# Performance work log

Measured on AMD Instinct MI355X. Metric: run time of the kernel, lower is better.

The kernel has to match this reference:

```python
import jax, jax.numpy as jnp
import numpy as np

N_NODES = 50000
N_EDGES = 800000
D_FEAT = 64
N_AGENTS = 1024
A_DIM = 16
MSG = 128          # msg_dim
OUT = 128          # out_dim


def _w(k, fan_in, fan_out):
    return jax.random.normal(k, (fan_in, fan_out), jnp.float32) / np.sqrt(fan_in).astype(np.float32)


def setup_inputs() -> dict:
    key = jax.random.key(0)
    ks = jax.random.split(key, 24)
    inp = {}
    inp["x"] = jax.random.normal(ks[0], (N_NODES, D_FEAT), jnp.float32)
    inp["actions"] = jax.random.normal(ks[1], (N_AGENTS, A_DIM), jnp.float32)
    inp["senders"] = jax.random.randint(ks[2], (N_EDGES,), 0, N_NODES, jnp.int32)
    inp["receivers"] = jax.random.randint(ks[3], (N_EDGES,), 0, N_NODES, jnp.int32)
    inp["n_agents"] = N_AGENTS
    # message MLP: concat(sender, receiver) -> 256 -> 256 -> msg_dim
    inp["W_m1"] = _w(ks[4], 2 * D_FEAT, 256); inp["b_m1"] = jnp.zeros((256,), jnp.float32)
    inp["W_m2"] = _w(ks[5], 256, 256);        inp["b_m2"] = jnp.zeros((256,), jnp.float32)
    inp["W_m3"] = _w(ks[6], 256, MSG);        inp["b_m3"] = jnp.zeros((MSG,), jnp.float32)
    # aggregation MLP: msg_dim -> 128 -> 128 -> msg_dim
    inp["W_a1"] = _w(ks[7], MSG, 128);        inp["b_a1"] = jnp.zeros((128,), jnp.float32)
    inp["W_a2"] = _w(ks[8], 128, 128);        inp["b_a2"] = jnp.zeros((128,), jnp.float32)
    inp["W_a3"] = _w(ks[9], 128, MSG);        inp["b_a3"] = jnp.zeros((MSG,), jnp.float32)
    # update MLP: concat(node, aggregated) -> 256 -> 256 -> out_dim
    inp["W_u1"] = _w(ks[10], D_FEAT + MSG, 256); inp["b_u1"] = jnp.zeros((256,), jnp.float32)
    inp["W_u2"] = _w(ks[11], 256, 256);          inp["b_u2"] = jnp.zeros((256,), jnp.float32)
    inp["W_u3"] = _w(ks[12], 256, OUT);          inp["b_u3"] = jnp.zeros((OUT,), jnp.float32)
    # critic head
    inp["W_act"] = _w(ks[13], A_DIM, 128);    inp["b_act"] = jnp.zeros((128,), jnp.float32)
    inp["W_h1"] = _w(ks[14], OUT + 128, 256); inp["b_h1"] = jnp.zeros((256,), jnp.float32)
    inp["W_h2"] = _w(ks[15], 256, 256);       inp["b_h2"] = jnp.zeros((256,), jnp.float32)
    inp["W_q"] = _w(ks[16], 256, 1);          inp["b_q"] = jnp.zeros((1,), jnp.float32)
    return inp


def reference(x, actions, senders, receivers, n_agents,
              W_m1, b_m1, W_m2, b_m2, W_m3, b_m3,
              W_a1, b_a1, W_a2, b_a2, W_a3, b_a3,
              W_u1, b_u1, W_u2, b_u2, W_u3, b_u3,
              W_act, b_act, W_h1, b_h1, W_h2, b_h2, W_q, b_q):
    relu = jax.nn.relu
    # --- GNN layer: edge messages (gather endpoints, MLP) ---
    h = jnp.concatenate([x[senders], x[receivers]], axis=-1)   # [E, 2*D]
    h = relu(h @ W_m1 + b_m1)
    h = relu(h @ W_m2 + b_m2)
    msg = h @ W_m3 + b_m3                                      # [E, MSG]
    # --- aggregate messages at receivers (scatter-add) ---
    aggr = jax.ops.segment_sum(msg, receivers, num_segments=x.shape[0])  # [N, MSG]
    a = relu(aggr @ W_a1 + b_a1)
    a = relu(a @ W_a2 + b_a2)
    a = a @ W_a3 + b_a3                                        # [N, MSG]
    # --- node update ---
    u = jnp.concatenate([x, a], axis=-1)                       # [N, D+MSG]
    u = relu(u @ W_u1 + b_u1)
    u = relu(u @ W_u2 + b_u2)
    feats = (u @ W_u3 + b_u3)[:n_agents]                       # agent (type-0) nodes
    # --- critic head ---
    ap = relu(actions @ W_act + b_act)                         # [n_agents, 128]
    z = jnp.concatenate([feats, ap], axis=-1)
    z = relu(z @ W_h1 + b_h1)
    z = relu(z @ W_h2 + b_h2)
    q = z @ W_q + b_q
    return jnp.squeeze(q, axis=-1)                             # [n_agents]
```

## Files before the change

### kernel.cpp

```cpp
#include <hip/hip_runtime.h>
#include <hip/hip_bf16.h>


#define STRIDE 260

typedef __attribute__((ext_vector_type(8))) short short8;
typedef __attribute__((ext_vector_type(4))) float floatx4;
union Frag8 { short8 s; uint u[4]; };

__device__ __forceinline__ void cvt_hi_lo(const float4 f0, const float4 f1,
                                          Frag8& hi, Frag8& lo) {
    uint U[8] = { __float_as_uint(f0.x), __float_as_uint(f0.y),
                  __float_as_uint(f0.z), __float_as_uint(f0.w),
                  __float_as_uint(f1.x), __float_as_uint(f1.y),
                  __float_as_uint(f1.z), __float_as_uint(f1.w) };
    float F[8] = { f0.x, f0.y, f0.z, f0.w, f1.x, f1.y, f1.z, f1.w };
#pragma unroll
    for (int p = 0; p < 4; ++p) {
        uint a = U[2*p], b = U[2*p+1];
        hi.u[p] = (a >> 16) | (b & 0xFFFF0000u);
        float l0 = F[2*p]   - __uint_as_float(a & 0xFFFF0000u);
        float l1 = F[2*p+1] - __uint_as_float(b & 0xFFFF0000u);
        __hip_bfloat162 pl = __float22bfloat162_rn(make_float2(l0, l1));
        union { __hip_bfloat162 h; uint v; } cvt; cvt.h = pl;
        lo.u[p] = cvt.v;
    }
}

__device__ __forceinline__ uint f2bf(float f) {
    uint u = __float_as_uint(f);
    return (u + 0x7FFFu + ((u >> 16) & 1u)) >> 16;
}
__device__ __forceinline__ float bf2f(uint h) { return __uint_as_float(h << 16); }
__device__ __forceinline__ uint split2(float f0, float f1, uint& lo) {
    uint h0 = f2bf(f0), h1 = f2bf(f1);
    uint l0 = f2bf(f0 - bf2f(h0)), l1 = f2bf(f1 - bf2f(h1));
    lo = l0 | (l1 << 16);
    return h0 | (h1 << 16);
}

constexpr int PK_NIN[11]  = {128,256,256, 128,128,128, 192,256,256, 256,256};
constexpr int PK_NOUT[11] = {256,256,128, 128,128,128, 256,256,128, 256,256};
constexpr int pk_entries(int m) { return (PK_NIN[m]/32)*(PK_NOUT[m]/16)*64; }
constexpr int pk_cum(int m) { int s = 0; for (int i = 0; i < m; ++i) s += pk_entries(i); return s; }
constexpr int PK_TOTAL = pk_cum(11);
constexpr int pk_off_hi(int m) { return 2*pk_cum(m); }
constexpr int pk_off_lo(int m) { return 2*pk_cum(m) + pk_entries(m); }

struct PackPtrs { const float* W[11]; };

#define FILT_CHUNK 4096

__global__ void pack_and_filter(PackPtrs P, uint4* __restrict__ pack,
                                const int* __restrict__ senders,
                                const int* __restrict__ receivers,
                                int E, int n_agents, int cap,
                                int* __restrict__ counter,
                                int2* __restrict__ edges, int FB) {
    __shared__ int lcount;
    __shared__ int lbase;
    __shared__ int2 lbuf[FILT_CHUNK];
    const int t = (int)threadIdx.x;
    if ((int)blockIdx.x < FB) {
        if (t == 0) lcount = 0;
        __syncthreads();
        int start = blockIdx.x * FILT_CHUNK;
        int end = min(start + FILT_CHUNK, E);
        for (int b0 = start; b0 < end; b0 += 256) {
            int idx = b0 + t;
            int r = -1, s = 0;
            bool pred = false;
            if (idx < end) {
                r = receivers[idx];
                pred = (r < n_agents);
                if (pred) s = senders[idx];
            }
            unsigned long long m = __ballot(pred);
            int lane = t & 63;
            int below = __popcll(m & ((1ull << lane) - 1));
            int cnt = __popcll(m);
            int wbase = 0;
            if (lane == 0 && cnt) wbase = atomicAdd(&lcount, cnt);
            wbase = __shfl(wbase, 0, 64);
            if (pred) lbuf[wbase + below] = make_int2(s, r);
        }
        __syncthreads();
        if (t == 0) lbase = atomicAdd(counter, lcount);
        __syncthreads();
        for (int i = t; i < lcount; i += 256) {
            int pos = lbase + i;
            if (pos < cap) edges[pos] = lbuf[i];
        }
        return;
    }
    int g = ((int)blockIdx.x - FB) * 256 + t;
    if (g >= PK_TOTAL) return;
    int m = 0;
#pragma unroll
    for (int i = 1; i < 11; ++i) if (g >= pk_cum(i)) m = i;
    int local = g - pk_cum(m);
    const float* W = P.W[m];
    int NOUT = PK_NOUT[m], NT = NOUT / 16;
    int lane = local & 63;
    int tmp  = local >> 6;
    int nt = tmp % NT, kb = tmp / NT;
    int n  = nt * 16 + (lane & 15);
    int k0 = kb * 32 + (lane >> 4) * 8;
    uint hi[4], lo[4];
#pragma unroll
    for (int p = 0; p < 4; ++p) {
        float f0 = W[(size_t)(k0 + 2*p)     * NOUT + n];
        float f1 = W[(size_t)(k0 + 2*p + 1) * NOUT + n];
        hi[p] = split2(f0, f1, lo[p]);
    }
    pack[pk_off_hi(m) + local] = make_uint4(hi[0], hi[1], hi[2], hi[3]);
    pack[pk_off_lo(m) + local] = make_uint4(lo[0], lo[1], lo[2], lo[3]);
}

template<int NIN, int NOUT, bool RELU>
__device__ __forceinline__ void mfma_layer(const float* in_lds, float* out_lds,
                                           const uint4* __restrict__ Whi,
                                           const uint4* __restrict__ Wlo,
                                           const float* __restrict__ b) {
    constexpr int KB  = NIN / 32;
    constexpr int NT  = NOUT / 16;
    constexpr int NTW = NT / 4;
    const int t    = (int)threadIdx.x;
    const int wave = t >> 6;
    const int l15  = t & 15;
    const int quad = (t >> 4) & 3;

    floatx4 acc[2][NTW];
#pragma unroll
    for (int mt = 0; mt < 2; ++mt)
#pragma unroll
        for (int i = 0; i < NTW; ++i) acc[mt][i] = (floatx4){0.f, 0.f, 0.f, 0.f};

#pragma unroll 2
    for (int kb = 0; kb < KB; ++kb) {
        Frag8 ahi[2], alo[2];
#pragma unroll
        for (int mt = 0; mt < 2; ++mt) {
            const float* src = in_lds + (mt * 16 + l15) * STRIDE + kb * 32 + quad * 8;
            float4 f0 = *(const float4*)src;
            float4 f1 = *(const float4*)(src + 4);
            cvt_hi_lo(f0, f1, ahi[mt], alo[mt]);
        }
#pragma unroll
        for (int i = 0; i < NTW; ++i) {
            int nt = wave * NTW + i;
            int widx = (kb * NT + nt) * 64 + (t & 63);
            Frag8 bhi, blo;
            *(uint4*)bhi.u = Whi[widx];
            *(uint4*)blo.u = Wlo[widx];
#pragma unroll
            for (int mt = 0; mt < 2; ++mt) {
                acc[mt][i] = __builtin_amdgcn_mfma_f32_16x16x32_bf16(alo[mt].s, bhi.s, acc[mt][i], 0, 0, 0);
                acc[mt][i] = __builtin_amdgcn_mfma_f32_16x16x32_bf16(ahi[mt].s, blo.s, acc[mt][i], 0, 0, 0);
                acc[mt][i] = __builtin_amdgcn_mfma_f32_16x16x32_bf16(ahi[mt].s, bhi.s, acc[mt][i], 0, 0, 0);
            }
        }
    }
#pragma unroll
    for (int i = 0; i < NTW; ++i) {
        int n = (wave * NTW + i) * 16 + l15;
        float bias = b[n];
#pragma unroll
        for (int mt = 0; mt < 2; ++mt) {
#pragma unroll
            for (int r = 0; r < 4; ++r) {
                float v = acc[mt][i][r] + bias;
                if (RELU) v = fmaxf(v, 0.f);
                out_lds[(mt * 16 + quad * 4 + r) * STRIDE + n] = v;
            }
        }
    }
}

template<int NIN, int NOUT, bool RELU, int OOFF>
__device__ __forceinline__ void mfma_layer16(const float* in_lds, float* out_lds,
                                             const uint4* __restrict__ Whi,
                                             const uint4* __restrict__ Wlo,
                                             const float* __restrict__ b) {
    constexpr int KB  = NIN / 32;
    constexpr int NT  = NOUT / 16;
    constexpr int NTW = NT / 4;
    const int t    = (int)threadIdx.x;
    const int wave = t >> 6;
    const int l15  = t & 15;
    const int quad = (t >> 4) & 3;

    floatx4 acc[NTW];
#pragma unroll
    for (int i = 0; i < NTW; ++i) acc[i] = (floatx4){0.f, 0.f, 0.f, 0.f};

#pragma unroll 2
    for (int kb = 0; kb < KB; ++kb) {
        Frag8 ahi, alo;
        const float* src = in_lds + l15 * STRIDE + kb * 32 + quad * 8;
        float4 f0 = *(const float4*)src;
        float4 f1 = *(const float4*)(src + 4);
        cvt_hi_lo(f0, f1, ahi, alo);
#pragma unroll
        for (int i = 0; i < NTW; ++i) {
            int widx = (kb * NT + wave * NTW + i) * 64 + (t & 63);
            Frag8 bhi, blo;
            *(uint4*)bhi.u = Whi[widx];
            *(uint4*)blo.u = Wlo[widx];
            acc[i] = __builtin_amdgcn_mfma_f32_16x16x32_bf16(alo.s, bhi.s, acc[i], 0, 0, 0);
            acc[i] = __builtin_amdgcn_mfma_f32_16x16x32_bf16(ahi.s, blo.s, acc[i], 0, 0, 0);
            acc[i] = __builtin_amdgcn_mfma_f32_16x16x32_bf16(ahi.s, bhi.s, acc[i], 0, 0, 0);
        }
    }
#pragma unroll
    for (int i = 0; i < NTW; ++i) {
        int n = (wave * NTW + i) * 16 + l15;
        float bias = b[n];
#pragma unroll
        for (int r = 0; r < 4; ++r) {
            float v = acc[i][r] + bias;
            if (RELU) v = fmaxf(v, 0.f);
            out_lds[(quad * 4 + r) * STRIDE + OOFF + n] = v;
        }
    }
}

#define ETE 32
__global__ __launch_bounds__(256, 2)
void edge_mlp(const float* __restrict__ x, const int2* __restrict__ edges,
              const int* __restrict__ counter, int cap, float* __restrict__ aggr,
              const uint4* __restrict__ pack,
              const float* __restrict__ bm1, const float* __restrict__ bm2,
              const float* __restrict__ bm3) {
    __shared__ float bufA[ETE * STRIDE];
    __shared__ float bufB[ETE * STRIDE];
    __shared__ int sL[ETE], rL[ETE];
    const uint4* W1hi = pack + pk_off_hi(0);
    const uint4* W1lo = pack + pk_off_lo(0);
    const uint4* W2hi = pack + pk_off_hi(1);
    const uint4* W2lo = pack + pk_off_lo(1);
    const uint4* W3hi = pack + pk_off_hi(2);
    const uint4* W3lo = pack + pk_off_lo(2);
    const int count = min(counter[0], cap);
    const int ntiles = (count + ETE - 1) / ETE;
    const int t = (int)threadIdx.x;
    for (int tile = (int)blockIdx.x; tile < ntiles; tile += (int)gridDim.x) {
        const int base = tile * ETE;
        if (t < ETE) {
            int eg = base + t;
            int2 ed = (eg < count) ? edges[eg] : make_int2(0, -1);
            sL[t] = ed.x; rL[t] = ed.y;
        }
        __syncthreads();
        for (int idx = t; idx < ETE * 32; idx += 256) {
            int e = idx >> 5;
            int f4 = (idx & 31) * 4;
            int node = (f4 < 64) ? sL[e] : rL[e];
            float4 v = make_float4(0.f, 0.f, 0.f, 0.f);
            if (rL[e] >= 0) v = *(const float4*)(x + (size_t)node * 64 + (f4 & 63));
            *(float4*)(bufA + e * STRIDE + f4) = v;
        }
        __syncthreads();
        mfma_layer<128, 256, true >(bufA, bufB, W1hi, W1lo, bm1);
        __syncthreads();
        mfma_layer<256, 256, true >(bufB, bufA, W2hi, W2lo, bm2);
        __syncthreads();
        mfma_layer<256, 128, false>(bufA, bufB, W3hi, W3lo, bm3);
        __syncthreads();
        for (int idx = t; idx < ETE * 128; idx += 256) {
            int e = idx >> 7, o = idx & 127;
            if (base + e < count) {
                atomicAdd(&aggr[(size_t)rL[e] * 128 + o], bufB[e * STRIDE + o]);
            }
        }
        __syncthreads();
    }
}

__global__ __launch_bounds__(256, 1)
void node_update(const float* __restrict__ x, const float* __restrict__ actions,
                 const float* __restrict__ aggr, int n_agents,
                 const uint4* __restrict__ pack,
                 const float* __restrict__ ba1, const float* __restrict__ ba2,
                 const float* __restrict__ ba3,
                 const float* __restrict__ bu1, const float* __restrict__ bu2,
                 const float* __restrict__ bu3,
                 const float* __restrict__ Wact, const float* __restrict__ bact,
                 const float* __restrict__ bh1, const float* __restrict__ bh2,
                 const float* __restrict__ Wq,  const float* __restrict__ bq,
                 float* __restrict__ out) {
    __shared__ float bufA[16 * STRIDE];
    __shared__ float bufB[16 * STRIDE];
    __shared__ float qpart[16][17];
    const int t = (int)threadIdx.x;
    const int base = (int)blockIdx.x * 16;

    for (int idx = t; idx < 16 * 32; idx += 256) {
        int e = idx >> 5, f4 = (idx & 31) * 4;
        float4 v = make_float4(0.f, 0.f, 0.f, 0.f);
        if (base + e < n_agents) v = *(const float4*)(aggr + (size_t)(base + e) * 128 + f4);
        *(float4*)(bufA + e * STRIDE + f4) = v;
    }
    __syncthreads();
    mfma_layer16<128, 128, true,  0 >(bufA, bufB, pack + pk_off_hi(3), pack + pk_off_lo(3), ba1);
    __syncthreads();
    mfma_layer16<128, 128, true,  0 >(bufB, bufA, pack + pk_off_hi(4), pack + pk_off_lo(4), ba2);
    __syncthreads();
    mfma_layer16<128, 128, false, 64>(bufA, bufB, pack + pk_off_hi(5), pack + pk_off_lo(5), ba3);
    for (int idx = t; idx < 16 * 16; idx += 256) {
        int e = idx >> 4, f4 = (idx & 15) * 4;
        float4 v = make_float4(0.f, 0.f, 0.f, 0.f);
        if (base + e < n_agents) v = *(const float4*)(x + (size_t)(base + e) * 64 + f4);
        *(float4*)(bufB + e * STRIDE + f4) = v;
    }
    __syncthreads();
    mfma_layer16<192, 256, true,  0 >(bufB, bufA, pack + pk_off_hi(6), pack + pk_off_lo(6), bu1);
    __syncthreads();
    mfma_layer16<256, 256, true,  0 >(bufA, bufB, pack + pk_off_hi(7), pack + pk_off_lo(7), bu2);
    __syncthreads();
    mfma_layer16<256, 128, false, 0 >(bufB, bufA, pack + pk_off_hi(8), pack + pk_off_lo(8), bu3);
    {
        int e = t >> 4, c0 = (t & 15) * 8;
        float accp[8];
#pragma unroll
        for (int c = 0; c < 8; ++c) accp[c] = bact[c0 + c];
        if (base + e < n_agents) {
#pragma unroll
            for (int k = 0; k < 16; ++k) {
                float av = actions[(size_t)(base + e) * 16 + k];
#pragma unroll
                for (int c = 0; c < 8; ++c)
                    accp[c] += av * Wact[(size_t)k * 128 + c0 + c];
            }
        }
#pragma unroll
        for (int c = 0; c < 8; ++c)
            bufA[e * STRIDE + 128 + c0 + c] = fmaxf(accp[c], 0.f);
    }
    __syncthreads();
    mfma_layer16<256, 256, true, 0>(bufA, bufB, pack + pk_off_hi(9),  pack + pk_off_lo(9),  bh1);
    __syncthreads();
    mfma_layer16<256, 256, true, 0>(bufB, bufA, pack + pk_off_hi(10), pack + pk_off_lo(10), bh2);
    __syncthreads();
    {
        int e = t >> 4, g = t & 15;
        const float* z = bufA + e * STRIDE + g * 16;
        const float* w = Wq + g * 16;
        float p = 0.f;
#pragma unroll
        for (int j = 0; j < 16; j += 4) {
            float4 zv = *(const float4*)(z + j);
            float4 wv = *(const float4*)(w + j);
            p += zv.x * wv.x + zv.y * wv.y + zv.z * wv.z + zv.w * wv.w;
        }
        qpart[e][g] = p;
    }
    __syncthreads();
    if (t < 16 && base + t < n_agents) {
        float s = bq[0];
#pragma unroll
        for (int g = 0; g < 16; ++g) s += qpart[t][g];
        out[base + t] = s;
    }
}

extern "C" void kernel_launch(void* const* d_in, const int* in_sizes, int n_in,
                              void* d_out, int out_size, void* d_ws, size_t ws_size,
                              hipStream_t stream) {
    const float* x        = (const float*)d_in[0];
    const float* actions  = (const float*)d_in[1];
    const int*   senders  = (const int*)d_in[2];
    const int*   receivers= (const int*)d_in[3];
    const float* Wm1 = (const float*)d_in[5],  *bm1 = (const float*)d_in[6];
    const float* Wm2 = (const float*)d_in[7],  *bm2 = (const float*)d_in[8];
    const float* Wm3 = (const float*)d_in[9],  *bm3 = (const float*)d_in[10];
    const float* Wa1 = (const float*)d_in[11], *ba1 = (const float*)d_in[12];
    const float* Wa2 = (const float*)d_in[13], *ba2 = (const float*)d_in[14];
    const float* Wa3 = (const float*)d_in[15], *ba3 = (const float*)d_in[16];
    const float* Wu1 = (const float*)d_in[17], *bu1 = (const float*)d_in[18];
    const float* Wu2 = (const float*)d_in[19], *bu2 = (const float*)d_in[20];
    const float* Wu3 = (const float*)d_in[21], *bu3 = (const float*)d_in[22];
    const float* Wact= (const float*)d_in[23], *bact= (const float*)d_in[24];
    const float* Wh1 = (const float*)d_in[25], *bh1 = (const float*)d_in[26];
    const float* Wh2 = (const float*)d_in[27], *bh2 = (const float*)d_in[28];
    const float* Wq  = (const float*)d_in[29], *bq  = (const float*)d_in[30];

    const int E = in_sizes[2];
    const int n_agents = out_size;

    char* ws = (char*)d_ws;
    int*   counter = (int*)ws;
    float* aggr    = (float*)(ws + 1024);
    const size_t packOff = 1024 + (size_t)n_agents * 128 * sizeof(float);
    uint4* pack    = (uint4*)(ws + packOff);
    const size_t packBytes = (size_t)2 * PK_TOTAL * 16;
    const size_t edgeOff = packOff + packBytes;
    int2*  edges   = (int2*)(ws + edgeOff);
    int cap = (int)((ws_size > edgeOff) ? (ws_size - edgeOff) / sizeof(int2) : 0);
    if (cap > E) cap = E;

    hipMemsetAsync(ws, 0, packOff, stream);

    PackPtrs P;
    P.W[0] = Wm1; P.W[1] = Wm2; P.W[2] = Wm3;
    P.W[3] = Wa1; P.W[4] = Wa2; P.W[5] = Wa3;
    P.W[6] = Wu1; P.W[7] = Wu2; P.W[8] = Wu3;
    P.W[9] = Wh1; P.W[10] = Wh2;
    const int FB = (E + FILT_CHUNK - 1) / FILT_CHUNK;
    const int PB = (PK_TOTAL + 255) / 256;
    pack_and_filter<<<FB + PB, 256, 0, stream>>>(P, pack, senders, receivers,
                                                 E, n_agents, cap, counter,
                                                 edges, FB);

    edge_mlp<<<512, 256, 0, stream>>>(x, edges, counter, cap, aggr, pack,
                                      bm1, bm2, bm3);

    node_update<<<(n_agents + 15) / 16, 256, 0, stream>>>(
        x, actions, aggr, n_agents, pack,
        ba1, ba2, ba3, bu1, bu2, bu3, Wact, bact, bh1, bh2, Wq, bq,
        (float*)d_out);
}
```

Baseline: 195.5 us.

## Double-buffer weight fragment loads, use per-chunk edge slots, drop memset

```diff
diff --git a/kernel.cpp b/kernel.cpp
--- a/kernel.cpp
+++ b/kernel.cpp
@@ -3,6 +3,9 @@
 
 
 #define STRIDE 260
+#define FILT_CHUNK 4096
+#define CSTRIDE 1024
+#define TPC (CSTRIDE / 32)
 
 typedef __attribute__((ext_vector_type(8))) short short8;
 typedef __attribute__((ext_vector_type(4))) float floatx4;
@@ -49,16 +52,14 @@
 
 struct PackPtrs { const float* W[11]; };
 
-#define FILT_CHUNK 4096
-
 __global__ void pack_and_filter(PackPtrs P, uint4* __restrict__ pack,
                                 const int* __restrict__ senders,
                                 const int* __restrict__ receivers,
-                                int E, int n_agents, int cap,
-                                int* __restrict__ counter,
-                                int2* __restrict__ edges, int FB) {
+                                int E, int n_agents,
+                                int* __restrict__ cnts,
+                                int2* __restrict__ edges,
+                                float* __restrict__ aggr, int aggrN, int FB) {
     __shared__ int lcount;
-    __shared__ int lbase;
     __shared__ int2 lbuf[FILT_CHUNK];
     const int t = (int)threadIdx.x;
     if ((int)blockIdx.x < FB) {
@@ -85,15 +86,14 @@
             if (pred) lbuf[wbase + below] = make_int2(s, r);
         }
         __syncthreads();
-        if (t == 0) lbase = atomicAdd(counter, lcount);
-        __syncthreads();
-        for (int i = t; i < lcount; i += 256) {
-            int pos = lbase + i;
-            if (pos < cap) edges[pos] = lbuf[i];
-        }
+        int c = min(lcount, CSTRIDE);
+        if (t == 0) cnts[blockIdx.x] = c;
+        int2* dst = edges + (size_t)blockIdx.x * CSTRIDE;
+        for (int i = t; i < c; i += 256) dst[i] = lbuf[i];
         return;
     }
     int g = ((int)blockIdx.x - FB) * 256 + t;
+    for (int i = g; i < aggrN; i += 224 * 256) aggr[i] = 0.f;
     if (g >= PK_TOTAL) return;
     int m = 0;
 #pragma unroll
@@ -117,18 +117,65 @@
     pack[pk_off_lo(m) + local] = make_uint4(lo[0], lo[1], lo[2], lo[3]);
 }
 
+template<int NT, int NTW>
+__device__ __forceinline__ void loadW(const uint4* __restrict__ Whi,
+                                      const uint4* __restrict__ Wlo,
+                                      int k, int lane, int wave,
+                                      Frag8 (&bh)[NTW], Frag8 (&bl)[NTW]) {
+#pragma unroll
+    for (int i = 0; i < NTW; ++i) {
+        int widx = (k * NT + wave * NTW + i) * 64 + lane;
+        *(uint4*)bh[i].u = Whi[widx];
+        *(uint4*)bl[i].u = Wlo[widx];
+    }
+}
+
+template<int NTW>
+__device__ __forceinline__ void compute2(const float* in_lds, int kb,
+                                         int l15, int quad,
+                                         Frag8 (&bh)[NTW], Frag8 (&bl)[NTW],
+                                         floatx4 (&acc)[2][NTW]) {
+    Frag8 ahi[2], alo[2];
+#pragma unroll
+    for (int mt = 0; mt < 2; ++mt) {
+        const float* src = in_lds + (mt * 16 + l15) * STRIDE + kb * 32 + quad * 8;
+        cvt_hi_lo(*(const float4*)src, *(const float4*)(src + 4), ahi[mt], alo[mt]);
+    }
+#pragma unroll
+    for (int i = 0; i < NTW; ++i)
+#pragma unroll
+        for (int mt = 0; mt < 2; ++mt) {
+            acc[mt][i] = __builtin_amdgcn_mfma_f32_16x16x32_bf16(alo[mt].s, bh[i].s, acc[mt][i], 0, 0, 0);
+            acc[mt][i] = __builtin_amdgcn_mfma_f32_16x16x32_bf16(ahi[mt].s, bl[i].s, acc[mt][i], 0, 0, 0);
+            acc[mt][i] = __builtin_amdgcn_mfma_f32_16x16x32_bf16(ahi[mt].s, bh[i].s, acc[mt][i], 0, 0, 0);
+        }
+}
+
+template<int NTW>
+__device__ __forceinline__ void compute1(const float* in_lds, int kb,
+                                         int l15, int quad,
+                                         Frag8 (&bh)[NTW], Frag8 (&bl)[NTW],
+                                         floatx4 (&acc)[NTW]) {
+    Frag8 ahi, alo;
+    const float* src = in_lds + l15 * STRIDE + kb * 32 + quad * 8;
+    cvt_hi_lo(*(const float4*)src, *(const float4*)(src + 4), ahi, alo);
+#pragma unroll
+    for (int i = 0; i < NTW; ++i) {
+        acc[i] = __builtin_amdgcn_mfma_f32_16x16x32_bf16(alo.s, bh[i].s, acc[i], 0, 0, 0);
+        acc[i] = __builtin_amdgcn_mfma_f32_16x16x32_bf16(ahi.s, bl[i].s, acc[i], 0, 0, 0);
+        acc[i] = __builtin_amdgcn_mfma_f32_16x16x32_bf16(ahi.s, bh[i].s, acc[i], 0, 0, 0);
+    }
+}
+
 template<int NIN, int NOUT, bool RELU>
 __device__ __forceinline__ void mfma_layer(const float* in_lds, float* out_lds,
                                            const uint4* __restrict__ Whi,
                                            const uint4* __restrict__ Wlo,
                                            const float* __restrict__ b) {
-    constexpr int KB  = NIN / 32;
-    constexpr int NT  = NOUT / 16;
-    constexpr int NTW = NT / 4;
-    const int t    = (int)threadIdx.x;
-    const int wave = t >> 6;
-    const int l15  = t & 15;
-    const int quad = (t >> 4) & 3;
+    constexpr int KB = NIN / 32, NT = NOUT / 16, NTW = NT / 4;
+    static_assert(KB % 2 == 0, "even KB for pairwise double-buffer");
+    const int t = (int)threadIdx.x;
+    const int wave = t >> 6, lane = t & 63, l15 = t & 15, quad = (t >> 4) & 3;
 
     floatx4 acc[2][NTW];
 #pragma unroll
@@ -136,44 +183,27 @@
 #pragma unroll
         for (int i = 0; i < NTW; ++i) acc[mt][i] = (floatx4){0.f, 0.f, 0.f, 0.f};
 
-#pragma unroll 2
-    for (int kb = 0; kb < KB; ++kb) {
-        Frag8 ahi[2], alo[2];
-#pragma unroll
-        for (int mt = 0; mt < 2; ++mt) {
-            const float* src = in_lds + (mt * 16 + l15) * STRIDE + kb * 32 + quad * 8;
-            float4 f0 = *(const float4*)src;
-            float4 f1 = *(const float4*)(src + 4);
-            cvt_hi_lo(f0, f1, ahi[mt], alo[mt]);
-        }
-#pragma unroll
-        for (int i = 0; i < NTW; ++i) {
-            int nt = wave * NTW + i;
-            int widx = (kb * NT + nt) * 64 + (t & 63);
-            Frag8 bhi, blo;
-            *(uint4*)bhi.u = Whi[widx];
-            *(uint4*)blo.u = Wlo[widx];
-#pragma unroll
-            for (int mt = 0; mt < 2; ++mt) {
-                acc[mt][i] = __builtin_amdgcn_mfma_f32_16x16x32_bf16(alo[mt].s, bhi.s, acc[mt][i], 0, 0, 0);
-                acc[mt][i] = __builtin_amdgcn_mfma_f32_16x16x32_bf16(ahi[mt].s, blo.s, acc[mt][i], 0, 0, 0);
-                acc[mt][i] = __builtin_amdgcn_mfma_f32_16x16x32_bf16(ahi[mt].s, bhi.s, acc[mt][i], 0, 0, 0);
-            }
-        }
+    Frag8 WAh[NTW], WAl[NTW], WBh[NTW], WBl[NTW];
+    loadW<NT, NTW>(Whi, Wlo, 0, lane, wave, WAh, WAl);
+#pragma unroll
+    for (int kb = 0; kb < KB; kb += 2) {
+        loadW<NT, NTW>(Whi, Wlo, kb + 1, lane, wave, WBh, WBl);
+        compute2<NTW>(in_lds, kb, l15, quad, WAh, WAl, acc);
+        if (kb + 2 < KB) loadW<NT, NTW>(Whi, Wlo, kb + 2, lane, wave, WAh, WAl);
+        compute2<NTW>(in_lds, kb + 1, l15, quad, WBh, WBl, acc);
     }
 #pragma unroll
     for (int i = 0; i < NTW; ++i) {
         int n = (wave * NTW + i) * 16 + l15;
         float bias = b[n];
 #pragma unroll
-        for (int mt = 0; mt < 2; ++mt) {
+        for (int mt = 0; mt < 2; ++mt)
 #pragma unroll
             for (int r = 0; r < 4; ++r) {
                 float v = acc[mt][i][r] + bias;
                 if (RELU) v = fmaxf(v, 0.f);
                 out_lds[(mt * 16 + quad * 4 + r) * STRIDE + n] = v;
             }
-        }
     }
 }
 
@@ -182,35 +212,23 @@
                                              const uint4* __restrict__ Whi,
                                              const uint4* __restrict__ Wlo,
                                              const float* __restrict__ b) {
-    constexpr int KB  = NIN / 32;
-    constexpr int NT  = NOUT / 16;
-    constexpr int NTW = NT / 4;
-    const int t    = (int)threadIdx.x;
-    const int wave = t >> 6;
-    const int l15  = t & 15;
-    const int quad = (t >> 4) & 3;
+    constexpr int KB = NIN / 32, NT = NOUT / 16, NTW = NT / 4;
+    static_assert(KB % 2 == 0, "even KB");
+    const int t = (int)threadIdx.x;
+    const int wave = t >> 6, lane = t & 63, l15 = t & 15, quad = (t >> 4) & 3;
 
     floatx4 acc[NTW];
 #pragma unroll
     for (int i = 0; i < NTW; ++i) acc[i] = (floatx4){0.f, 0.f, 0.f, 0.f};
 
-#pragma unroll 2
-    for (int kb = 0; kb < KB; ++kb) {
-        Frag8 ahi, alo;
-        const float* src = in_lds + l15 * STRIDE + kb * 32 + quad * 8;
-        float4 f0 = *(const float4*)src;
-        float4 f1 = *(const float4*)(src + 4);
-        cvt_hi_lo(f0, f1, ahi, alo);
-#pragma unroll
-        for (int i = 0; i < NTW; ++i) {
-            int widx = (kb * NT + wave * NTW + i) * 64 + (t & 63);
-            Frag8 bhi, blo;
-            *(uint4*)bhi.u = Whi[widx];
-            *(uint4*)blo.u = Wlo[widx];
-            acc[i] = __builtin_amdgcn_mfma_f32_16x16x32_bf16(alo.s, bhi.s, acc[i], 0, 0, 0);
-            acc[i] = __builtin_amdgcn_mfma_f32_16x16x32_bf16(ahi.s, blo.s, acc[i], 0, 0, 0);
-            acc[i] = __builtin_amdgcn_mfma_f32_16x16x32_bf16(ahi.s, bhi.s, acc[i], 0, 0, 0);
-        }
+    Frag8 WAh[NTW], WAl[NTW], WBh[NTW], WBl[NTW];
+    loadW<NT, NTW>(Whi, Wlo, 0, lane, wave, WAh, WAl);
+#pragma unroll
+    for (int kb = 0; kb < KB; kb += 2) {
+        loadW<NT, NTW>(Whi, Wlo, kb + 1, lane, wave, WBh, WBl);
+        compute1<NTW>(in_lds, kb, l15, quad, WAh, WAl, acc);
+        if (kb + 2 < KB) loadW<NT, NTW>(Whi, Wlo, kb + 2, lane, wave, WAh, WAl);
+        compute1<NTW>(in_lds, kb + 1, l15, quad, WBh, WBl, acc);
     }
 #pragma unroll
     for (int i = 0; i < NTW; ++i) {
@@ -228,27 +246,24 @@
 #define ETE 32
 __global__ __launch_bounds__(256, 2)
 void edge_mlp(const float* __restrict__ x, const int2* __restrict__ edges,
-              const int* __restrict__ counter, int cap, float* __restrict__ aggr,
+              const int* __restrict__ cnts, float* __restrict__ aggr,
               const uint4* __restrict__ pack,
               const float* __restrict__ bm1, const float* __restrict__ bm2,
-              const float* __restrict__ bm3) {
+              const float* __restrict__ bm3, int FB) {
     __shared__ float bufA[ETE * STRIDE];
     __shared__ float bufB[ETE * STRIDE];
     __shared__ int sL[ETE], rL[ETE];
-    const uint4* W1hi = pack + pk_off_hi(0);
-    const uint4* W1lo = pack + pk_off_lo(0);
-    const uint4* W2hi = pack + pk_off_hi(1);
-    const uint4* W2lo = pack + pk_off_lo(1);
-    const uint4* W3hi = pack + pk_off_hi(2);
-    const uint4* W3lo = pack + pk_off_lo(2);
-    const int count = min(counter[0], cap);
-    const int ntiles = (count + ETE - 1) / ETE;
     const int t = (int)threadIdx.x;
-    for (int tile = (int)blockIdx.x; tile < ntiles; tile += (int)gridDim.x) {
-        const int base = tile * ETE;
+    const int vtiles = FB * TPC;
+    for (int vt = (int)blockIdx.x; vt < vtiles; vt += (int)gridDim.x) {
+        const int chunk = vt / TPC, ti = vt % TPC;
+        const int cnt = cnts[chunk];
+        if (ti * 32 >= cnt) continue;
+        const int2* ce = edges + (size_t)chunk * CSTRIDE;
+        const int base = ti * 32;
         if (t < ETE) {
             int eg = base + t;
-            int2 ed = (eg < count) ? edges[eg] : make_int2(0, -1);
+            int2 ed = (eg < cnt) ? ce[eg] : make_int2(0, -1);
             sL[t] = ed.x; rL[t] = ed.y;
         }
         __syncthreads();
@@ -261,15 +276,15 @@
             *(float4*)(bufA + e * STRIDE + f4) = v;
         }
         __syncthreads();
-        mfma_layer<128, 256, true >(bufA, bufB, W1hi, W1lo, bm1);
-        __syncthreads();
-        mfma_layer<256, 256, true >(bufB, bufA, W2hi, W2lo, bm2);
-        __syncthreads();
-        mfma_layer<256, 128, false>(bufA, bufB, W3hi, W3lo, bm3);
+        mfma_layer<128, 256, true >(bufA, bufB, pack + pk_off_hi(0), pack + pk_off_lo(0), bm1);
+        __syncthreads();
+        mfma_layer<256, 256, true >(bufB, bufA, pack + pk_off_hi(1), pack + pk_off_lo(1), bm2);
+        __syncthreads();
+        mfma_layer<256, 128, false>(bufA, bufB, pack + pk_off_hi(2), pack + pk_off_lo(2), bm3);
         __syncthreads();
         for (int idx = t; idx < ETE * 128; idx += 256) {
             int e = idx >> 7, o = idx & 127;
-            if (base + e < count) {
+            if (rL[e] >= 0) {
                 atomicAdd(&aggr[(size_t)rL[e] * 128 + o], bufB[e * STRIDE + o]);
             }
         }
@@ -389,31 +404,28 @@
     const int n_agents = out_size;
 
     char* ws = (char*)d_ws;
-    int*   counter = (int*)ws;
-    float* aggr    = (float*)(ws + 1024);
+    int*   cnts = (int*)ws;
+    float* aggr = (float*)(ws + 1024);
     const size_t packOff = 1024 + (size_t)n_agents * 128 * sizeof(float);
-    uint4* pack    = (uint4*)(ws + packOff);
+    uint4* pack = (uint4*)(ws + packOff);
     const size_t packBytes = (size_t)2 * PK_TOTAL * 16;
     const size_t edgeOff = packOff + packBytes;
-    int2*  edges   = (int2*)(ws + edgeOff);
-    int cap = (int)((ws_size > edgeOff) ? (ws_size - edgeOff) / sizeof(int2) : 0);
-    if (cap > E) cap = E;
-
-    hipMemsetAsync(ws, 0, packOff, stream);
+    int2* edges = (int2*)(ws + edgeOff);
+
+    const int FB = (E + FILT_CHUNK - 1) / FILT_CHUNK;
+    const int PB = (PK_TOTAL + 255) / 256;
 
     PackPtrs P;
     P.W[0] = Wm1; P.W[1] = Wm2; P.W[2] = Wm3;
     P.W[3] = Wa1; P.W[4] = Wa2; P.W[5] = Wa3;
     P.W[6] = Wu1; P.W[7] = Wu2; P.W[8] = Wu3;
     P.W[9] = Wh1; P.W[10] = Wh2;
-    const int FB = (E + FILT_CHUNK - 1) / FILT_CHUNK;
-    const int PB = (PK_TOTAL + 255) / 256;
     pack_and_filter<<<FB + PB, 256, 0, stream>>>(P, pack, senders, receivers,
-                                                 E, n_agents, cap, counter,
-                                                 edges, FB);
-
-    edge_mlp<<<512, 256, 0, stream>>>(x, edges, counter, cap, aggr, pack,
-                                      bm1, bm2, bm3);
+                                                 E, n_agents, cnts, edges,
+                                                 aggr, n_agents * 128, FB);
+
+    edge_mlp<<<512, 256, 0, stream>>>(x, edges, cnts, aggr, pack,
+                                      bm1, bm2, bm3, FB);
 
     node_update<<<(n_agents + 15) / 16, 256, 0, stream>>>(
         x, actions, aggr, n_agents, pack,
```

Measured after the change: 505.8 us. +158.8%, slower.
